# Optimization experiments

Hardware: AMD Instinct MI355X
Metric: run time of the kernel (lower is better)

## Reference

```python
import jax, jax.numpy as jnp
import numpy as np

# pywt db4 decomposition filters
DEC_LO = jnp.array([-0.010597401784997278, 0.032883011666982945, 0.030841381835986965, -0.18703481171888114, -0.02798376941698385, 0.6308807679295904, 0.7148465705525415, 0.23037781330885523], dtype=jnp.float32)
DEC_HI = jnp.array([-0.23037781330885523, 0.7148465705525415, -0.6308807679295904, -0.02798376941698385, 0.18703481171888114, 0.030841381835986965, -0.032883011666982945, -0.010597401784997278], dtype=jnp.float32)

def _dwt_step(x):
    # single-level DWT along last axis, pywt 'symmetric' mode; x: [N, n]
    L = DEC_LO.shape[0]
    xe = jnp.pad(x, ((0, 0), (L - 1, L - 1)), mode='symmetric')[:, 1:]
    k = jnp.stack([DEC_LO[::-1], DEC_HI[::-1]])[:, None, :]  # [2,1,L]
    y = jax.lax.conv_general_dilated(xe[:, None, :], k, window_strides=(2,), padding='VALID')
    return y[:, 0, :], y[:, 1, :]  # cA, cD, each [N, (n+L-1)//2]

def _wavedec(x, level):
    a, dets = x, []
    for _ in range(level):
        a, d = _dwt_step(a)
        dets.append(d)
    return [a] + dets[::-1]  # [cA_L, cD_L, ..., cD_1]

def _wavelet_kan(x, basis, scales=5):
    # torch code detaches x before pywt.wavedec -> stop_gradient for faithful bwd
    coeffs = _wavedec(jax.lax.stop_gradient(x), scales - 1)
    out = 0.0
    for s in range(scales):
        c = coeffs[s]
        out = out + c @ basis[s][:c.shape[1], :]
    return out

def _dendritic(x, W, b):
    # W: [branches, in, out]; max over branches of GELU(Linear)
    h = jnp.einsum('ni,kio->kno', x, W) + b[:, None, :]
    return jnp.max(jax.nn.gelu(h, approximate=False), axis=0)

def _layernorm(x, g, b, eps=1e-5):
    m = jnp.mean(x, -1, keepdims=True)
    v = jnp.var(x, -1, keepdims=True)
    return (x - m) * jax.lax.rsqrt(v + eps) * g + b

def setup_inputs():
    key = jax.random.key(0)
    ks = jax.random.split(key, 12)
    N, D, H, M, Z, K, E = 16384, 768, 512, 256, 256, 20, 262144
    inp = {}
    inp['x'] = jax.random.normal(ks[0], (N, D), jnp.float32)
    inp['adj_rows'] = jax.random.randint(ks[1], (E,), 0, N, jnp.int32)
    inp['adj_cols'] = jax.random.randint(ks[2], (E,), 0, N, jnp.int32)
    inp['adj_vals'] = jax.random.uniform(ks[3], (E,), jnp.float32)
    inp['basis_enc'] = jax.random.normal(ks[4], (5, D, H), jnp.float32)
    inp['ln_g'] = jnp.ones((H,), jnp.float32)
    inp['ln_b'] = jnp.zeros((H,), jnp.float32)
    inp['Wd_enc'] = jax.random.normal(ks[5], (K, H, M), jnp.float32) * 0.04
    inp['bd_enc'] = jnp.zeros((K, M), jnp.float32)
    inp['W_mu'] = jax.random.normal(ks[6], (M, Z), jnp.float32) * 0.06
    inp['b_mu'] = jnp.zeros((Z,), jnp.float32)
    inp['W_lv'] = jax.random.normal(ks[7], (M, Z), jnp.float32) * 0.06
    inp['b_lv'] = jnp.zeros((Z,), jnp.float32)
    inp['Wd_dec'] = jax.random.normal(ks[8], (K, Z, H), jnp.float32) * 0.06
    inp['bd_dec'] = jnp.zeros((K, H), jnp.float32)
    inp['basis_dec'] = jax.random.normal(ks[9], (5, H, D), jnp.float32)
    inp['eps'] = jax.random.normal(ks[10], (N, Z), jnp.float32)
    return inp

def reference(x, adj_rows, adj_cols, adj_vals, basis_enc, ln_g, ln_b, Wd_enc, bd_enc, W_mu, b_mu, W_lv, b_lv, Wd_dec, bd_dec, basis_dec, eps):
    N = x.shape[0]
    # torch.sparse.mm(adj, x) with COO adj
    xa = jax.ops.segment_sum(adj_vals[:, None] * x[adj_cols], adj_rows, num_segments=N)
    h = _wavelet_kan(xa, basis_enc)
    h = _layernorm(h, ln_g, ln_b)
    enc = _dendritic(h, Wd_enc, bd_enc)
    mu = enc @ W_mu + b_mu
    logvar = enc @ W_lv + b_lv
    z = mu + eps * jnp.exp(0.5 * logvar)
    dec = _dendritic(z, Wd_dec, bd_dec)
    recon = _wavelet_kan(dec, basis_dec)
    return recon, mu, logvar
```

## Files before the change

### kernel.cpp

```cpp
#include <hip/hip_runtime.h>

typedef __attribute__((ext_vector_type(8))) short short8v;
typedef __attribute__((ext_vector_type(8))) unsigned short ushort8v;
typedef __attribute__((ext_vector_type(4))) float float4v;

__device__ __constant__ float c_LO[8] = {
    -0.010597401784997278f, 0.032883011666982945f, 0.030841381835986965f,
    -0.18703481171888114f, -0.02798376941698385f, 0.6308807679295904f,
    0.7148465705525415f, 0.23037781330885523f};
__device__ __constant__ float c_HI[8] = {
    -0.23037781330885523f, 0.7148465705525415f, -0.6308807679295904f,
    -0.02798376941698385f, 0.18703481171888114f, 0.030841381835986965f,
    -0.032883011666982945f, -0.010597401784997278f};

__device__ __forceinline__ unsigned short f2bf(float f) {
    unsigned u = __builtin_bit_cast(unsigned, f);
    unsigned r = u + 0x7fffu + ((u >> 16) & 1u);
    return (unsigned short)(r >> 16);
}
__device__ __forceinline__ float bf2f(unsigned short u) {
    return __builtin_bit_cast(float, (unsigned)u << 16);
}

__device__ __forceinline__ float gelu_fast(float x) {
    float x3 = x * x * x;
    float y = fmaf(0.044715f, x3, x) * 0.7978845608028654f;
    float t = fminf(fmaxf(y * 2.8853900817779268f, -30.f), 30.f);
    float e = exp2f(t);
    return x * e * __builtin_amdgcn_rcpf(e + 1.0f);
}

__device__ __forceinline__ void gload_lds16(const void* g, void* l) {
    __builtin_amdgcn_global_load_lds(g, l, 16, 0, 0);
}

__device__ __forceinline__ void dwt_lvl(const float* __restrict__ in, int n, float* __restrict__ outA,
                                        unsigned short* __restrict__ outD, int m, int lane) {
    for (int j = lane; j < m; j += 64) {
        float a = 0.f, d = 0.f;
#pragma unroll
        for (int i = 0; i < 8; ++i) {
            int p = 2 * j + 7 - i;
            int q = (p < 6) ? (5 - p) : ((p < n + 6) ? (p - 6) : (2 * n + 5 - p));
            float xv = in[q];
            a = fmaf(c_LO[i], xv, a);
            d = fmaf(c_HI[i], xv, d);
        }
        outA[j] = a;
        outD[j] = f2bf(d);
    }
}
__device__ __forceinline__ void dwt_lvl_final(const float* __restrict__ in, int n, unsigned short* __restrict__ outA,
                                              unsigned short* __restrict__ outD, int m, int lane) {
    for (int j = lane; j < m; j += 64) {
        float a = 0.f, d = 0.f;
#pragma unroll
        for (int i = 0; i < 8; ++i) {
            int p = 2 * j + 7 - i;
            int q = (p < 6) ? (5 - p) : ((p < n + 6) ? (p - 6) : (2 * n + 5 - p));
            float xv = in[q];
            a = fmaf(c_LO[i], xv, a);
            d = fmaf(c_HI[i], xv, d);
        }
        outA[j] = f2bf(a);
        outD[j] = f2bf(d);
    }
}

__global__ void hist_kernel(const int* __restrict__ rows, int* __restrict__ cnt, int E) {
    int i = blockIdx.x * blockDim.x + threadIdx.x;
    if (i < E) atomicAdd(&cnt[rows[i]], 1);
}

__global__ __launch_bounds__(1024) void scan_kernel(const int* __restrict__ cnt, int* __restrict__ offs,
                                                    int* __restrict__ cursor, int Nrows, int E) {
    __shared__ int part[1024];
    int tid = threadIdx.x;
    const int per = Nrows / 1024;
    int base = tid * per;
    int local[16];
    int s = 0;
    for (int i = 0; i < per; ++i) { local[i] = s; s += cnt[base + i]; }
    part[tid] = s;
    __syncthreads();
    for (int off = 1; off < 1024; off <<= 1) {
        int v = part[tid];
        int w = (tid >= off) ? part[tid - off] : 0;
        __syncthreads();
        part[tid] = v + w;
        __syncthreads();
    }
    int pre = (tid == 0) ? 0 : part[tid - 1];
    for (int i = 0; i < per; ++i) {
        int o = pre + local[i];
        offs[base + i] = o;
        cursor[base + i] = o;
    }
    if (tid == 0) offs[Nrows] = E;
}

__global__ void scatter_kernel(const int* __restrict__ rows, const int* __restrict__ cols,
                               const float* __restrict__ vals, int* __restrict__ cursor,
                               int* __restrict__ ccol, float* __restrict__ cval, int E) {
    int i = blockIdx.x * blockDim.x + threadIdx.x;
    if (i >= E) return;
    int r = rows[i];
    int p = atomicAdd(&cursor[r], 1);
    ccol[p] = cols[i];
    cval[p] = vals[i];
}

__global__ __launch_bounds__(256) void wavedec_enc_x(const float* __restrict__ x,
                                                     unsigned short* __restrict__ cenc) {
    __shared__ float buf0[4][768];
    __shared__ float buf1[4][400];
    const int widx = threadIdx.x >> 6, lane = threadIdx.x & 63;
    const int r = blockIdx.x * 4 + widx;
    float* b0 = buf0[widx];
    float* b1 = buf1[widx];
    const float* ip = x + (size_t)r * 768;
    for (int i = lane; i < 768; i += 64) b0[i] = ip[i];
    __syncthreads();
    unsigned short* cr = cenc + (size_t)r * 800;
    dwt_lvl(b0, 768, b1, cr + 407, 387, lane);
    __syncthreads();
    dwt_lvl(b1, 387, b0, cr + 210, 197, lane);
    __syncthreads();
    dwt_lvl(b0, 197, b1, cr + 108, 102, lane);
    __syncthreads();
    dwt_lvl_final(b1, 102, cr + 0, cr + 54, 54, lane);
    if (lane < 6) cr[794 + lane] = 0;
}

__global__ __launch_bounds__(256) void spmm_ln(const unsigned short* __restrict__ hx,
                                               const int* __restrict__ offs,
                                               const int* __restrict__ ccol,
                                               const float* __restrict__ cval,
                                               const float* __restrict__ g,
                                               const float* __restrict__ b,
                                               unsigned short* __restrict__ hbf) {
    const int widx = threadIdx.x >> 6, lane = threadIdx.x & 63;
    const int r = blockIdx.x * 4 + widx;
    int s = offs[r], e = offs[r + 1];
    float acc[8] = {};
    for (int j = s; j < e; ++j) {
        int c = ccol[j];
        float v = cval[j];
        ushort8v u = *(const ushort8v*)(hx + (size_t)c * 512 + lane * 8);
#pragma unroll
        for (int t = 0; t < 8; ++t) acc[t] = fmaf(v, bf2f(u[t]), acc[t]);
    }
    float s1 = 0.f, s2 = 0.f;
#pragma unroll
    for (int t = 0; t < 8; ++t) { s1 += acc[t]; s2 = fmaf(acc[t], acc[t], s2); }
#pragma unroll
    for (int off = 32; off >= 1; off >>= 1) {
        s1 += __shfl_xor(s1, off);
        s2 += __shfl_xor(s2, off);
    }
    float mean = s1 * (1.f / 512.f);
    float var = s2 * (1.f / 512.f) - mean * mean;
    float inv = rsqrtf(var + 1e-5f);
    ushort8v o;
#pragma unroll
    for (int t = 0; t < 8; ++t) {
        int col = lane * 8 + t;
        o[t] = f2bf((acc[t] - mean) * inv * g[col] + b[col]);
    }
    *(ushort8v*)(hbf + (size_t)r * 512 + lane * 8) = o;
}

__global__ __launch_bounds__(256) void wavedec_dec(const unsigned short* __restrict__ decb,
                                                   unsigned short* __restrict__ cdec) {
    __shared__ float buf0[4][512];
    __shared__ float buf1[4][272];
    const int widx = threadIdx.x >> 6, lane = threadIdx.x & 63;
    const int r = blockIdx.x * 4 + widx;
    float* b0 = buf0[widx];
    float* b1 = buf1[widx];
    const unsigned short* ip = decb + (size_t)r * 512;
    for (int i = lane; i < 512; i += 64) b0[i] = bf2f(ip[i]);
    __syncthreads();
    unsigned short* cr = cdec + (size_t)r * 544;
    dwt_lvl(b0, 512, b1, cr + 279, 259, lane);
    __syncthreads();
    dwt_lvl(b1, 259, b0, cr + 146, 133, lane);
    __syncthreads();
    dwt_lvl(b0, 133, b1, cr + 76, 70, lane);
    __syncthreads();
    dwt_lvl_final(b1, 70, cr + 0, cr + 38, 38, lane);
    if (lane < 6) cr[538 + lane] = 0;
}

struct Bounds { int b[6]; };

__global__ __launch_bounds__(256) void pack_wT_t(const float* __restrict__ W, unsigned short* __restrict__ WT,
                                                 int K, int N, int Kpad) {
    __shared__ float t[64][65];
    const int b = blockIdx.z;
    const int k0 = blockIdx.x * 64, n0 = blockIdx.y * 64;
    const int tid = threadIdx.x;
#pragma unroll
    for (int i = 0; i < 16; ++i) {
        int idx = tid + i * 256;
        int kk = idx >> 6, nn = idx & 63;
        int k = k0 + kk;
        t[kk][nn] = (k < K) ? W[((size_t)b * K + k) * N + n0 + nn] : 0.f;
    }
    __syncthreads();
#pragma unroll
    for (int i = 0; i < 16; ++i) {
        int idx = tid + i * 256;
        int nn = idx >> 6, kk = idx & 63;
        int k = k0 + kk;
        if (k < Kpad)
            WT[((size_t)b * N + n0 + nn) * Kpad + k] = f2bf(t[kk][nn]);
    }
}

__global__ __launch_bounds__(256) void pack_basis_t(const float* __restrict__ basis, unsigned short* __restrict__ BT,
                                                    Bounds bd, int brows, int N, int K, int Kpad) {
    __shared__ float t[64][65];
    const int k0 = blockIdx.x * 64, n0 = blockIdx.y * 64;
    const int tid = threadIdx.x;
#pragma unroll
    for (int i = 0; i < 16; ++i) {
        int idx = tid + i * 256;
        int kk = idx >> 6, nn = idx & 63;
        int k = k0 + kk;
        float v = 0.f;
        if (k < K) {
            int s = 0;
#pragma unroll
            for (int u = 1; u < 5; ++u)
                if (k >= bd.b[u]) s = u;
            int lr = k - bd.b[s];
            v = basis[((size_t)s * brows + lr) * N + n0 + nn];
        }
        t[kk][nn] = v;
    }
    __syncthreads();
#pragma unroll
    for (int i = 0; i < 16; ++i) {
        int idx = tid + i * 256;
        int nn = idx >> 6, kk = idx & 63;
        int k = k0 + kk;
        if (k < Kpad)
            BT[(size_t)(n0 + nn) * Kpad + k] = f2bf(t[kk][nn]);
    }
}

template <int MODE>
__global__ __launch_bounds__(256) void gemm_mfma(const unsigned short* __restrict__ A,
                                                 const unsigned short* __restrict__ BT,
                                                 const float* __restrict__ bias,
                                                 const float* __restrict__ bias2,
                                                 void* __restrict__ Cv, void* __restrict__ Cv2,
                                                 int M, int N, int K, int lda, int ldb, int ldc, int nx) {
    __shared__ __align__(16) unsigned short As[128 * 32];
    __shared__ __align__(16) unsigned short Bs[128 * 32];
    const int tid = threadIdx.x;
    const int wave = tid >> 6, lane = tid & 63;
    const int nwg = gridDim.x;
    const int logical = (blockIdx.x & 7) * (nwg >> 3) + (blockIdx.x >> 3);
    const int mblk = logical / nx, nblk = logical - mblk * nx;
    const int m0 = mblk * 128, n0 = nblk * 128;
    const int wr = wave >> 1, wc = wave & 1;
    const int frow = lane & 15, fq = lane >> 4;

    const int off0 = tid * 16;
    const int r0 = off0 >> 6, c0 = off0 & 63;
    const int r1 = (off0 + 4096) >> 6, c1 = (off0 + 4096) & 63;
    const char* Ab = (const char*)A;
    const char* Bb = (const char*)BT;
    size_t gA0 = (size_t)(m0 + r0) * lda * 2 + c0;
    size_t gA1 = (size_t)(m0 + r1) * lda * 2 + c1;
    size_t gB0 = (size_t)(n0 + r0) * ldb * 2 + c0;
    size_t gB1 = (size_t)(n0 + r1) * ldb * 2 + c1;
    char* lA0 = (char*)As + wave * 1024;
    char* lB0 = (char*)Bs + wave * 1024;

    const int aoff = (wr * 64 + frow) * 32 + fq * 8;
    const int boff = (wc * 64 + frow) * 32 + fq * 8;

    float4v acc[4][4] = {};
    for (int k0 = 0; k0 < K; k0 += 32) {
        size_t kb2 = (size_t)k0 * 2;
        gload_lds16(Ab + gA0 + kb2, lA0);
        gload_lds16(Ab + gA1 + kb2, lA0 + 4096);
        gload_lds16(Bb + gB0 + kb2, lB0);
        gload_lds16(Bb + gB1 + kb2, lB0 + 4096);
        __syncthreads();
        short8v av[4], bv[4];
#pragma unroll
        for (int i = 0; i < 4; ++i) av[i] = *(const short8v*)(As + aoff + i * 512);
#pragma unroll
        for (int i = 0; i < 4; ++i) bv[i] = *(const short8v*)(Bs + boff + i * 512);
#pragma unroll
        for (int mi = 0; mi < 4; ++mi)
#pragma unroll
            for (int ni = 0; ni < 4; ++ni)
                acc[mi][ni] = __builtin_amdgcn_mfma_f32_16x16x32_bf16(av[mi], bv[ni], acc[mi][ni], 0, 0, 0);
        __syncthreads();
    }
#pragma unroll
    for (int ni = 0; ni < 4; ++ni) {
        int col = n0 + wc * 64 + ni * 16 + frow;
#pragma unroll
        for (int mi = 0; mi < 4; ++mi) {
#pragma unroll
            for (int i = 0; i < 4; ++i) {
                int row = m0 + wr * 64 + mi * 16 + fq * 4 + i;
                if (MODE == 0) {
                    ((float*)Cv)[(size_t)row * ldc + col] = acc[mi][ni][i];
                } else if (MODE == 1) {
                    ((unsigned short*)Cv)[(size_t)row * ldc + col] = f2bf(acc[mi][ni][i]);
                } else {
                    bool isMu = col < 256;
                    int coll = col & 255;
                    float bval = isMu ? bias[coll] : bias2[coll];
                    float* dst = (float*)(isMu ? Cv : Cv2);
                    dst[(size_t)row * 256 + coll] = acc[mi][ni][i] + bval;
                }
            }
        }
    }
}

__global__ void z_kernel(const float* __restrict__ mu, const float* __restrict__ lv,
                         const float* __restrict__ eps, unsigned short* __restrict__ z, int n4) {
    int i = blockIdx.x * blockDim.x + threadIdx.x;
    if (i >= n4) return;
    float4 m = ((const float4*)mu)[i];
    float4 l = ((const float4*)lv)[i];
    float4 e = ((const float4*)eps)[i];
    ushort4 o;
    o.x = f2bf(m.x + e.x * expf(0.5f * l.x));
    o.y = f2bf(m.y + e.y * expf(0.5f * l.y));
    o.z = f2bf(m.z + e.z * expf(0.5f * l.z));
    o.w = f2bf(m.w + e.w * expf(0.5f * l.w));
    ((ushort4*)z)[i] = o;
}

__global__ __launch_bounds__(256, 2) void dendritic_full(const unsigned short* __restrict__ A,
                                                         const unsigned short* __restrict__ WT,
                                                         const float* __restrict__ bias,
                                                         unsigned short* __restrict__ out,
                                                         int M, int Nc, int K, int nb, int nx) {
    __shared__ __align__(16) unsigned short As[128 * 64];
    __shared__ __align__(16) unsigned short Bs[2][64 * 64];
    const int tid = threadIdx.x;
    const int wave = tid >> 6;
    const int lane = tid & 63;

    const int nwg = gridDim.x;
    const int logical = (blockIdx.x & 7) * (nwg >> 3) + (blockIdx.x >> 3);
    const int mblk = logical / nx;
    const int nblk = logical - mblk * nx;
    const int n0 = nblk * 64, m0 = mblk * 128;

    const int wr = wave >> 1, wc = wave & 1;
    const int frow = lane & 15, fq = lane >> 4;

    int srA[4], scA[4];
#pragma unroll
    for (int i = 0; i < 4; ++i) {
        int ch = i * 256 + tid;
        srA[i] = ch >> 3;
        scA[i] = ((ch & 7) ^ (srA[i] & 7)) * 16;
    }
    int srB[2], scB[2];
#pragma unroll
    for (int i = 0; i < 2; ++i) {
        int ch = i * 256 + tid;
        srB[i] = ch >> 3;
        scB[i] = ((ch & 7) ^ (srB[i] & 7)) * 16;
    }
    const char* Ab = (const char*)A;
    const size_t K2 = (size_t)K * 2;
    const size_t branchBytes = (size_t)Nc * K2;
    char* lA  = (char*)As + wave * 1024;
    char* lB0 = (char*)&Bs[0][0] + wave * 1024;
    char* lB1 = (char*)&Bs[1][0] + wave * 1024;

    float4v hmn[4][2], hmx[4][2];
#pragma unroll
    for (int mi = 0; mi < 4; ++mi)
#pragma unroll
        for (int ni = 0; ni < 2; ++ni) { hmn[mi][ni] = (float4v)(1e30f); hmx[mi][ni] = (float4v)(-1e30f); }

    const int npair = nb >> 1;
    for (int p = 0; p < npair; ++p) {
        const int b0 = 2 * p, b1 = 2 * p + 1;
        const char* Bb0 = (const char*)WT + (size_t)b0 * branchBytes;
        const char* Bb1 = (const char*)WT + (size_t)b1 * branchBytes;
        float4v ac0[4][2], ac1[4][2];
#pragma unroll
        for (int ni = 0; ni < 2; ++ni) {
            int col = n0 + wc * 32 + ni * 16 + frow;
            float bv0 = bias[(size_t)b0 * Nc + col];
            float bv1 = bias[(size_t)b1 * Nc + col];
#pragma unroll
            for (int mi = 0; mi < 4; ++mi) { ac0[mi][ni] = (float4v)(bv0); ac1[mi][ni] = (float4v)(bv1); }
        }
        for (int k0 = 0; k0 < K; k0 += 64) {
            const size_t kby = (size_t)k0 * 2;
#pragma unroll
            for (int i = 0; i < 4; ++i)
                gload_lds16(Ab + (size_t)(m0 + srA[i]) * K2 + kby + scA[i], lA + i * 4096);
#pragma unroll
            for (int i = 0; i < 2; ++i)
                gload_lds16(Bb0 + (size_t)(n0 + srB[i]) * K2 + kby + scB[i], lB0 + i * 4096);
#pragma unroll
            for (int i = 0; i < 2; ++i)
                gload_lds16(Bb1 + (size_t)(n0 + srB[i]) * K2 + kby + scB[i], lB1 + i * 4096);
            __syncthreads();
#pragma unroll
            for (int kk = 0; kk < 2; ++kk) {
                short8v av[4], bv0[2], bv1[2];
                const int slot = kk * 4 + fq;
#pragma unroll
                for (int mi = 0; mi < 4; ++mi) {
                    int ra = wr * 64 + mi * 16 + frow;
                    av[mi] = *(const short8v*)((const char*)As + ra * 128 + ((slot ^ (ra & 7)) * 16));
                }
#pragma unroll
                for (int ni = 0; ni < 2; ++ni) {
                    int rb = wc * 32 + ni * 16 + frow;
                    int rboff = rb * 128 + ((slot ^ (rb & 7)) * 16);
                    bv0[ni] = *(const short8v*)((const char*)&Bs[0][0] + rboff);
                    bv1[ni] = *(const short8v*)((const char*)&Bs[1][0] + rboff);
                }
#pragma unroll
                for (int mi = 0; mi < 4; ++mi)
#pragma unroll
                    for (int ni = 0; ni < 2; ++ni) {
                        ac0[mi][ni] = __builtin_amdgcn_mfma_f32_16x16x32_bf16(av[mi], bv0[ni], ac0[mi][ni], 0, 0, 0);
                        ac1[mi][ni] = __builtin_amdgcn_mfma_f32_16x16x32_bf16(av[mi], bv1[ni], ac1[mi][ni], 0, 0, 0);
                    }
            }
            __syncthreads();
        }
#pragma unroll
        for (int ni = 0; ni < 2; ++ni)
#pragma unroll
            for (int mi = 0; mi < 4; ++mi)
#pragma unroll
                for (int i = 0; i < 4; ++i) {
                    float mn = fminf(ac0[mi][ni][i], ac1[mi][ni][i]);
                    float mx = fmaxf(ac0[mi][ni][i], ac1[mi][ni][i]);
                    hmn[mi][ni][i] = fminf(hmn[mi][ni][i], mn);
                    hmx[mi][ni][i] = fmaxf(hmx[mi][ni][i], mx);
                }
    }

#pragma unroll
    for (int ni = 0; ni < 2; ++ni) {
        int col = n0 + wc * 32 + ni * 16 + frow;
#pragma unroll
        for (int mi = 0; mi < 4; ++mi) {
#pragma unroll
            for (int i = 0; i < 4; ++i) {
                int row = m0 + wr * 64 + mi * 16 + fq * 4 + i;
                float g = fmaxf(gelu_fast(hmn[mi][ni][i]), gelu_fast(hmx[mi][ni][i]));
                out[(size_t)row * Nc + col] = f2bf(g);
            }
        }
    }
}

__global__ __launch_bounds__(256, 2) void dendritic_dec_res(const unsigned short* __restrict__ A,
                                                            const unsigned short* __restrict__ WT,
                                                            const float* __restrict__ bias,
                                                            unsigned short* __restrict__ out,
                                                            int M, int Nc, int nb, int nx) {
    constexpr int K = 256;
    __shared__ __align__(16) unsigned short As[128 * 256];
    __shared__ __align__(16) unsigned short Bs[2][64 * 64];
    const int tid = threadIdx.x;
    const int wave = tid >> 6;
    const int lane = tid & 63;

    const int nwg = gridDim.x;
    const int logical = (blockIdx.x & 7) * (nwg >> 3) + (blockIdx.x >> 3);
    const int mblk = logical / nx;
    const int nblk = logical - mblk * nx;
    const int n0 = nblk * 64, m0 = mblk * 128;

    const int wr = wave >> 1, wc = wave & 1;
    const int frow = lane & 15, fq = lane >> 4;

    const char* Ab = (const char*)A;
    const size_t K2 = (size_t)K * 2;
    for (int i = 0; i < 16; ++i) {
        int ch = i * 256 + tid;
        int row = ch >> 5, slot = ch & 31;
        int sslot = (slot & ~7) | ((slot & 7) ^ (row & 7));
        gload_lds16(Ab + (size_t)(m0 + row) * K2 + sslot * 16, (char*)As + i * 4096 + wave * 1024);
    }

    int srB[2], scB[2];
#pragma unroll
    for (int i = 0; i < 2; ++i) {
        int ch = i * 256 + tid;
        srB[i] = ch >> 3;
        scB[i] = ((ch & 7) ^ (srB[i] & 7)) * 16;
    }
    const size_t branchBytes = (size_t)Nc * K2;
    char* lB0 = (char*)&Bs[0][0] + wave * 1024;
    char* lB1 = (char*)&Bs[1][0] + wave * 1024;

    float4v hmn[4][2], hmx[4][2];
#pragma unroll
    for (int mi = 0; mi < 4; ++mi)
#pragma unroll
        for (int ni = 0; ni < 2; ++ni) { hmn[mi][ni] = (float4v)(1e30f); hmx[mi][ni] = (float4v)(-1e30f); }

    const int npair = nb >> 1;
    for (int p = 0; p < npair; ++p) {
        const int b0 = 2 * p, b1 = 2 * p + 1;
        const char* Bb0 = (const char*)WT + (size_t)b0 * branchBytes;
        const char* Bb1 = (const char*)WT + (size_t)b1 * branchBytes;
        float4v ac0[4][2], ac1[4][2];
#pragma unroll
        for (int ni = 0; ni < 2; ++ni) {
            int col = n0 + wc * 32 + ni * 16 + frow;
            float bv0 = bias[(size_t)b0 * Nc + col];
            float bv1 = bias[(size_t)b1 * Nc + col];
#pragma unroll
            for (int mi = 0; mi < 4; ++mi) { ac0[mi][ni] = (float4v)(bv0); ac1[mi][ni] = (float4v)(bv1); }
        }
        for (int k0 = 0; k0 < K; k0 += 64) {
            const size_t kby = (size_t)k0 * 2;
#pragma unroll
            for (int i = 0; i < 2; ++i)
                gload_lds16(Bb0 + (size_t)(n0 + srB[i]) * K2 + kby + scB[i], lB0 + i * 4096);
#pragma unroll
            for (int i = 0; i < 2; ++i)
                gload_lds16(Bb1 + (size_t)(n0 + srB[i]) * K2 + kby + scB[i], lB1 + i * 4096);
            __syncthreads();
#pragma unroll
            for (int kk = 0; kk < 2; ++kk) {
                short8v av[4], bv0[2], bv1[2];
                const int slot = kk * 4 + fq;
#pragma unroll
                for (int mi = 0; mi < 4; ++mi) {
                    int ra = wr * 64 + mi * 16 + frow;
                    int g = (k0 >> 3) + slot;
                    int sl = (g & ~7) | ((g & 7) ^ (ra & 7));
                    av[mi] = *(const short8v*)((const char*)As + ra * 512 + sl * 16);
                }
#pragma unroll
                for (int ni = 0; ni < 2; ++ni) {
                    int rb = wc * 32 + ni * 16 + frow;
                    int rboff = rb * 128 + ((slot ^ (rb & 7)) * 16);
                    bv0[ni] = *(const short8v*)((const char*)&Bs[0][0] + rboff);
                    bv1[ni] = *(const short8v*)((const char*)&Bs[1][0] + rboff);
                }
#pragma unroll
                for (int mi = 0; mi < 4; ++mi)
#pragma unroll
                    for (int ni = 0; ni < 2; ++ni) {
                        ac0[mi][ni] = __builtin_amdgcn_mfma_f32_16x16x32_bf16(av[mi], bv0[ni], ac0[mi][ni], 0, 0, 0);
                        ac1[mi][ni] = __builtin_amdgcn_mfma_f32_16x16x32_bf16(av[mi], bv1[ni], ac1[mi][ni], 0, 0, 0);
                    }
            }
            __syncthreads();
        }
#pragma unroll
        for (int ni = 0; ni < 2; ++ni)
#pragma unroll
            for (int mi = 0; mi < 4; ++mi)
#pragma unroll
                for (int i = 0; i < 4; ++i) {
                    float mn = fminf(ac0[mi][ni][i], ac1[mi][ni][i]);
                    float mx = fmaxf(ac0[mi][ni][i], ac1[mi][ni][i]);
                    hmn[mi][ni][i] = fminf(hmn[mi][ni][i], mn);
                    hmx[mi][ni][i] = fmaxf(hmx[mi][ni][i], mx);
                }
    }

#pragma unroll
    for (int ni = 0; ni < 2; ++ni) {
        int col = n0 + wc * 32 + ni * 16 + frow;
#pragma unroll
        for (int mi = 0; mi < 4; ++mi) {
#pragma unroll
            for (int i = 0; i < 4; ++i) {
                int row = m0 + wr * 64 + mi * 16 + fq * 4 + i;
                float g = fmaxf(gelu_fast(hmn[mi][ni][i]), gelu_fast(hmx[mi][ni][i]));
                out[(size_t)row * Nc + col] = f2bf(g);
            }
        }
    }
}

extern "C" void kernel_launch(void* const* d_in, const int* in_sizes, int n_in,
                              void* d_out, int out_size, void* d_ws, size_t ws_size,
                              hipStream_t stream) {
    const float* x        = (const float*)d_in[0];
    const int*   arows    = (const int*)d_in[1];
    const int*   acols    = (const int*)d_in[2];
    const float* avals    = (const float*)d_in[3];
    const float* basisenc = (const float*)d_in[4];
    const float* ln_g     = (const float*)d_in[5];
    const float* ln_b     = (const float*)d_in[6];
    const float* Wd_enc   = (const float*)d_in[7];
    const float* bd_enc   = (const float*)d_in[8];
    const float* W_mu     = (const float*)d_in[9];
    const float* b_mu     = (const float*)d_in[10];
    const float* W_lv     = (const float*)d_in[11];
    const float* b_lv     = (const float*)d_in[12];
    const float* Wd_dec   = (const float*)d_in[13];
    const float* bd_dec   = (const float*)d_in[14];
    const float* basisdec = (const float*)d_in[15];
    const float* epsin    = (const float*)d_in[16];

    const int N = 16384;
    const int E = in_sizes[1];

    float* ws = (float*)d_ws;
    const size_t A0 = 0;
    const size_t B0 = A0 + (size_t)N * 768;
    const size_t C0 = B0 + (size_t)N * 400;
    const size_t F0 = C0 + (size_t)N * 387;
    const size_t G0 = F0 + 3100672;

    unsigned short* hx   = (unsigned short*)(ws + A0);
    unsigned short* cenc = (unsigned short*)(ws + B0);
    unsigned short* cdec = (unsigned short*)(ws + B0);
    unsigned short* zb   = cdec + (size_t)N * 544;
    unsigned short* hbf  = (unsigned short*)(ws + C0);
    unsigned short* encb = hbf + (size_t)N * 512;
    unsigned short* decb = (unsigned short*)(ws + C0);
    unsigned short* wF = (unsigned short*)(ws + F0);
    unsigned short* BceT   = wF;
    unsigned short* BcdT   = BceT + 512 * 800;
    unsigned short* WdencT = BcdT + 768 * 544;
    unsigned short* WddecT = WdencT + 20 * 256 * 512;
    unsigned short* WmuT   = WddecT + 20 * 512 * 256;
    unsigned short* WlvT   = WmuT + 256 * 256;
    int*   csr_cnt  = (int*)(ws + G0);
    int*   csr_offs = csr_cnt + N;
    int*   csr_cur  = csr_offs + N + 1;
    int*   csr_col  = csr_cur + N;
    float* csr_val  = (float*)(csr_col + E);

    float* out_recon = (float*)d_out;
    float* out_mu    = out_recon + (size_t)N * 768;
    float* out_lv    = out_mu + (size_t)N * 256;

    {
        Bounds be = {{0, 54, 108, 210, 407, 794}};
        pack_basis_t<<<dim3(13, 8), 256, 0, stream>>>(basisenc, BceT, be, 768, 512, 794, 800);
        Bounds bdd = {{0, 38, 76, 146, 279, 538}};
        pack_basis_t<<<dim3(9, 12), 256, 0, stream>>>(basisdec, BcdT, bdd, 512, 768, 538, 544);
        pack_wT_t<<<dim3(8, 4, 20), 256, 0, stream>>>(Wd_enc, WdencT, 512, 256, 512);
        pack_wT_t<<<dim3(4, 8, 20), 256, 0, stream>>>(Wd_dec, WddecT, 256, 512, 256);
        pack_wT_t<<<dim3(4, 4, 1), 256, 0, stream>>>(W_mu, WmuT, 256, 256, 256);
        pack_wT_t<<<dim3(4, 4, 1), 256, 0, stream>>>(W_lv, WlvT, 256, 256, 256);
    }

    hipMemsetAsync(csr_cnt, 0, N * sizeof(int), stream);
    hist_kernel<<<(E + 255) / 256, 256, 0, stream>>>(arows, csr_cnt, E);
    scan_kernel<<<1, 1024, 0, stream>>>(csr_cnt, csr_offs, csr_cur, N, E);
    scatter_kernel<<<(E + 255) / 256, 256, 0, stream>>>(arows, acols, avals, csr_cur, csr_col, csr_val, E);
    wavedec_enc_x<<<N / 4, 256, 0, stream>>>(x, cenc);

    gemm_mfma<1><<<(512 / 128) * (N / 128), 256, 0, stream>>>(cenc, BceT, nullptr, nullptr, hx, nullptr,
                                                              N, 512, 800, 800, 800, 512, 512 / 128);

    spmm_ln<<<N / 4, 256, 0, stream>>>(hx, csr_offs, csr_col, csr_val, ln_g, ln_b, hbf);

    dendritic_full<<<4 * (N / 128), 256, 0, stream>>>(hbf, WdencT, bd_enc, encb, N, 256, 512, 20, 4);

    gemm_mfma<2><<<(512 / 128) * (N / 128), 256, 0, stream>>>(encb, WmuT, b_mu, b_lv, out_mu, out_lv,
                                                              N, 512, 256, 256, 256, 256, 512 / 128);

    z_kernel<<<(N * 256 / 4 + 255) / 256, 256, 0, stream>>>(out_mu, out_lv, epsin, zb, N * 256 / 4);

    dendritic_dec_res<<<8 * (N / 128), 256, 0, stream>>>(zb, WddecT, bd_dec, decb, N, 512, 20, 8);

    wavedec_dec<<<N / 4, 256, 0, stream>>>(decb, cdec);

    gemm_mfma<0><<<(768 / 128) * (N / 128), 256, 0, stream>>>(cdec, BcdT, nullptr, nullptr, out_recon, nullptr,
                                                              N, 768, 544, 544, 544, 768, 768 / 128);

    (void)ws_size; (void)out_size; (void)n_in;
}
```

Measured before the change: 457.3 us.

## Merge weight packing, encoder wavedec and histogram into one prep kernel; unroll SpMM

```diff
diff --git a/kernel.cpp b/kernel.cpp
--- a/kernel.cpp
+++ b/kernel.cpp
@@ -67,9 +67,123 @@
     }
 }
 
-__global__ void hist_kernel(const int* __restrict__ rows, int* __restrict__ cnt, int E) {
-    int i = blockIdx.x * blockDim.x + threadIdx.x;
-    if (i < E) atomicAdd(&cnt[rows[i]], 1);
+struct Bounds { int b[6]; };
+
+__device__ __forceinline__ void job_pack_w(const float* __restrict__ W, unsigned short* __restrict__ WT,
+                                           int br, int k0, int n0, int K, int N, int Kpad,
+                                           float (*t)[65], int tid) {
+#pragma unroll
+    for (int i = 0; i < 16; ++i) {
+        int idx = tid + i * 256;
+        int kk = idx >> 6, nn = idx & 63;
+        int k = k0 + kk;
+        t[kk][nn] = (k < K) ? W[((size_t)br * K + k) * N + n0 + nn] : 0.f;
+    }
+    __syncthreads();
+#pragma unroll
+    for (int i = 0; i < 16; ++i) {
+        int idx = tid + i * 256;
+        int nn = idx >> 6, kk = idx & 63;
+        int k = k0 + kk;
+        if (k < Kpad)
+            WT[((size_t)br * N + n0 + nn) * Kpad + k] = f2bf(t[kk][nn]);
+    }
+}
+
+__device__ __forceinline__ void job_pack_basis(const float* __restrict__ basis, unsigned short* __restrict__ BT,
+                                               Bounds bd, int brows, int N, int K, int Kpad,
+                                               int k0, int n0, float (*t)[65], int tid) {
+#pragma unroll
+    for (int i = 0; i < 16; ++i) {
+        int idx = tid + i * 256;
+        int kk = idx >> 6, nn = idx & 63;
+        int k = k0 + kk;
+        float v = 0.f;
+        if (k < K) {
+            int s = 0;
+#pragma unroll
+            for (int u = 1; u < 5; ++u)
+                if (k >= bd.b[u]) s = u;
+            int lr = k - bd.b[s];
+            v = basis[((size_t)s * brows + lr) * N + n0 + nn];
+        }
+        t[kk][nn] = v;
+    }
+    __syncthreads();
+#pragma unroll
+    for (int i = 0; i < 16; ++i) {
+        int idx = tid + i * 256;
+        int nn = idx >> 6, kk = idx & 63;
+        int k = k0 + kk;
+        if (k < Kpad)
+            BT[(size_t)(n0 + nn) * Kpad + k] = f2bf(t[kk][nn]);
+    }
+}
+
+__global__ __launch_bounds__(256) void prep_kernel(const float* __restrict__ x,
+                                                   const float* __restrict__ basisenc,
+                                                   const float* __restrict__ basisdec,
+                                                   const float* __restrict__ Wd_enc,
+                                                   const float* __restrict__ Wd_dec,
+                                                   const float* __restrict__ W_mu,
+                                                   const float* __restrict__ W_lv,
+                                                   const int* __restrict__ arows, int E,
+                                                   unsigned short* __restrict__ cenc,
+                                                   unsigned short* __restrict__ BceT,
+                                                   unsigned short* __restrict__ BcdT,
+                                                   unsigned short* __restrict__ WdencT,
+                                                   unsigned short* __restrict__ WddecT,
+                                                   unsigned short* __restrict__ WmuT,
+                                                   unsigned short* __restrict__ WlvT,
+                                                   int* __restrict__ csr_cnt) {
+    __shared__ __align__(16) char smem[18688];
+    const int bid = blockIdx.x;
+    const int tid = threadIdx.x;
+    float (*t)[65] = (float(*)[65])smem;
+
+    if (bid < 104) {
+        Bounds be = {{0, 54, 108, 210, 407, 794}};
+        int b = bid;
+        job_pack_basis(basisenc, BceT, be, 768, 512, 794, 800, (b % 13) * 64, (b / 13) * 64, t, tid);
+    } else if (bid < 212) {
+        Bounds bdd = {{0, 38, 76, 146, 279, 538}};
+        int b = bid - 104;
+        job_pack_basis(basisdec, BcdT, bdd, 512, 768, 538, 544, (b % 9) * 64, (b / 9) * 64, t, tid);
+    } else if (bid < 852) {
+        int b = bid - 212;
+        int br = b / 32, rem = b % 32;
+        job_pack_w(Wd_enc, WdencT, br, (rem % 8) * 64, (rem / 8) * 64, 512, 256, 512, t, tid);
+    } else if (bid < 1492) {
+        int b = bid - 852;
+        int br = b / 32, rem = b % 32;
+        job_pack_w(Wd_dec, WddecT, br, (rem % 4) * 64, (rem / 4) * 64, 256, 512, 256, t, tid);
+    } else if (bid < 1508) {
+        int b = bid - 1492;
+        job_pack_w(W_mu, WmuT, 0, (b % 4) * 64, (b / 4) * 64, 256, 256, 256, t, tid);
+    } else if (bid < 1524) {
+        int b = bid - 1508;
+        job_pack_w(W_lv, WlvT, 0, (b % 4) * 64, (b / 4) * 64, 256, 256, 256, t, tid);
+    } else if (bid < 5620) {
+        const int widx = tid >> 6, lane = tid & 63;
+        const int r = (bid - 1524) * 4 + widx;
+        float* b0 = (float*)smem + widx * 1168;
+        float* b1 = b0 + 768;
+        const float* ip = x + (size_t)r * 768;
+        for (int i = lane; i < 768; i += 64) b0[i] = ip[i];
+        __syncthreads();
+        unsigned short* cr = cenc + (size_t)r * 800;
+        dwt_lvl(b0, 768, b1, cr + 407, 387, lane);
+        __syncthreads();
+        dwt_lvl(b1, 387, b0, cr + 210, 197, lane);
+        __syncthreads();
+        dwt_lvl(b0, 197, b1, cr + 108, 102, lane);
+        __syncthreads();
+        dwt_lvl_final(b1, 102, cr + 0, cr + 54, 54, lane);
+        if (lane < 6) cr[794 + lane] = 0;
+    } else {
+        int i = (bid - 5620) * 256 + tid;
+        if (i < E) atomicAdd(&csr_cnt[arows[i]], 1);
+    }
 }
 
 __global__ __launch_bounds__(1024) void scan_kernel(const int* __restrict__ cnt, int* __restrict__ offs,
@@ -110,28 +224,6 @@
     cval[p] = vals[i];
 }
 
-__global__ __launch_bounds__(256) void wavedec_enc_x(const float* __restrict__ x,
-                                                     unsigned short* __restrict__ cenc) {
-    __shared__ float buf0[4][768];
-    __shared__ float buf1[4][400];
-    const int widx = threadIdx.x >> 6, lane = threadIdx.x & 63;
-    const int r = blockIdx.x * 4 + widx;
-    float* b0 = buf0[widx];
-    float* b1 = buf1[widx];
-    const float* ip = x + (size_t)r * 768;
-    for (int i = lane; i < 768; i += 64) b0[i] = ip[i];
-    __syncthreads();
-    unsigned short* cr = cenc + (size_t)r * 800;
-    dwt_lvl(b0, 768, b1, cr + 407, 387, lane);
-    __syncthreads();
-    dwt_lvl(b1, 387, b0, cr + 210, 197, lane);
-    __syncthreads();
-    dwt_lvl(b0, 197, b1, cr + 108, 102, lane);
-    __syncthreads();
-    dwt_lvl_final(b1, 102, cr + 0, cr + 54, 54, lane);
-    if (lane < 6) cr[794 + lane] = 0;
-}
-
 __global__ __launch_bounds__(256) void spmm_ln(const unsigned short* __restrict__ hx,
                                                const int* __restrict__ offs,
                                                const int* __restrict__ ccol,
@@ -142,14 +234,29 @@
     const int widx = threadIdx.x >> 6, lane = threadIdx.x & 63;
     const int r = blockIdx.x * 4 + widx;
     int s = offs[r], e = offs[r + 1];
-    float acc[8] = {};
-    for (int j = s; j < e; ++j) {
-        int c = ccol[j];
-        float v = cval[j];
-        ushort8v u = *(const ushort8v*)(hx + (size_t)c * 512 + lane * 8);
-#pragma unroll
-        for (int t = 0; t < 8; ++t) acc[t] = fmaf(v, bf2f(u[t]), acc[t]);
-    }
+    float acc[8] = {}, acc2[8] = {};
+    int j = s;
+    for (; j + 1 < e; j += 2) {
+        int c0 = ccol[j], c1 = ccol[j + 1];
+        float v0 = cval[j], v1 = cval[j + 1];
+        ushort8v u0 = *(const ushort8v*)(hx + (size_t)c0 * 512 + lane * 8);
+        ushort8v u1 = *(const ushort8v*)(hx + (size_t)c1 * 512 + lane * 8);
+#pragma unroll
+        for (int t = 0; t < 8; ++t) {
+            acc[t] = fmaf(v0, bf2f(u0[t]), acc[t]);
+            acc2[t] = fmaf(v1, bf2f(u1[t]), acc2[t]);
+        }
+    }
+    if (j < e) {
+        int c0 = ccol[j];
+        float v0 = cval[j];
+        ushort8v u0 = *(const ushort8v*)(hx + (size_t)c0 * 512 + lane * 8);
+#pragma unroll
+        for (int t = 0; t < 8; ++t) acc[t] = fmaf(v0, bf2f(u0[t]), acc[t]);
+    }
+#pragma unroll
+    for (int t = 0; t < 8; ++t) acc[t] += acc2[t];
+
     float s1 = 0.f, s2 = 0.f;
 #pragma unroll
     for (int t = 0; t < 8; ++t) { s1 += acc[t]; s2 = fmaf(acc[t], acc[t], s2); }
@@ -192,64 +299,6 @@
     if (lane < 6) cr[538 + lane] = 0;
 }
 
-struct Bounds { int b[6]; };
-
-__global__ __launch_bounds__(256) void pack_wT_t(const float* __restrict__ W, unsigned short* __restrict__ WT,
-                                                 int K, int N, int Kpad) {
-    __shared__ float t[64][65];
-    const int b = blockIdx.z;
-    const int k0 = blockIdx.x * 64, n0 = blockIdx.y * 64;
-    const int tid = threadIdx.x;
-#pragma unroll
-    for (int i = 0; i < 16; ++i) {
-        int idx = tid + i * 256;
-        int kk = idx >> 6, nn = idx & 63;
-        int k = k0 + kk;
-        t[kk][nn] = (k < K) ? W[((size_t)b * K + k) * N + n0 + nn] : 0.f;
-    }
-    __syncthreads();
-#pragma unroll
-    for (int i = 0; i < 16; ++i) {
-        int idx = tid + i * 256;
-        int nn = idx >> 6, kk = idx & 63;
-        int k = k0 + kk;
-        if (k < Kpad)
-            WT[((size_t)b * N + n0 + nn) * Kpad + k] = f2bf(t[kk][nn]);
-    }
-}
-
-__global__ __launch_bounds__(256) void pack_basis_t(const float* __restrict__ basis, unsigned short* __restrict__ BT,
-                                                    Bounds bd, int brows, int N, int K, int Kpad) {
-    __shared__ float t[64][65];
-    const int k0 = blockIdx.x * 64, n0 = blockIdx.y * 64;
-    const int tid = threadIdx.x;
-#pragma unroll
-    for (int i = 0; i < 16; ++i) {
-        int idx = tid + i * 256;
-        int kk = idx >> 6, nn = idx & 63;
-        int k = k0 + kk;
-        float v = 0.f;
-        if (k < K) {
-            int s = 0;
-#pragma unroll
-            for (int u = 1; u < 5; ++u)
-                if (k >= bd.b[u]) s = u;
-            int lr = k - bd.b[s];
-            v = basis[((size_t)s * brows + lr) * N + n0 + nn];
-        }
-        t[kk][nn] = v;
-    }
-    __syncthreads();
-#pragma unroll
-    for (int i = 0; i < 16; ++i) {
-        int idx = tid + i * 256;
-        int nn = idx >> 6, kk = idx & 63;
-        int k = k0 + kk;
-        if (k < Kpad)
-            BT[(size_t)(n0 + nn) * Kpad + k] = f2bf(t[kk][nn]);
-    }
-}
-
 template <int MODE>
 __global__ __launch_bounds__(256) void gemm_mfma(const unsigned short* __restrict__ A,
                                                  const unsigned short* __restrict__ BT,
@@ -650,22 +699,15 @@
     float* out_mu    = out_recon + (size_t)N * 768;
     float* out_lv    = out_mu + (size_t)N * 256;
 
+    hipMemsetAsync(csr_cnt, 0, N * sizeof(int), stream);
     {
-        Bounds be = {{0, 54, 108, 210, 407, 794}};
-        pack_basis_t<<<dim3(13, 8), 256, 0, stream>>>(basisenc, BceT, be, 768, 512, 794, 800);
-        Bounds bdd = {{0, 38, 76, 146, 279, 538}};
-        pack_basis_t<<<dim3(9, 12), 256, 0, stream>>>(basisdec, BcdT, bdd, 512, 768, 538, 544);
-        pack_wT_t<<<dim3(8, 4, 20), 256, 0, stream>>>(Wd_enc, WdencT, 512, 256, 512);
-        pack_wT_t<<<dim3(4, 8, 20), 256, 0, stream>>>(Wd_dec, WddecT, 256, 512, 256);
-        pack_wT_t<<<dim3(4, 4, 1), 256, 0, stream>>>(W_mu, WmuT, 256, 256, 256);
-        pack_wT_t<<<dim3(4, 4, 1), 256, 0, stream>>>(W_lv, WlvT, 256, 256, 256);
-    }
-
-    hipMemsetAsync(csr_cnt, 0, N * sizeof(int), stream);
-    hist_kernel<<<(E + 255) / 256, 256, 0, stream>>>(arows, csr_cnt, E);
+        const int nwgPrep = 104 + 108 + 640 + 640 + 16 + 16 + (N / 4) + (E + 255) / 256;
+        prep_kernel<<<nwgPrep, 256, 0, stream>>>(x, basisenc, basisdec, Wd_enc, Wd_dec, W_mu, W_lv,
+                                                 arows, E, cenc, BceT, BcdT, WdencT, WddecT, WmuT, WlvT,
+                                                 csr_cnt);
+    }
     scan_kernel<<<1, 1024, 0, stream>>>(csr_cnt, csr_offs, csr_cur, N, E);
     scatter_kernel<<<(E + 255) / 256, 256, 0, stream>>>(arows, acols, avals, csr_cur, csr_col, csr_val, E);
-    wavedec_enc_x<<<N / 4, 256, 0, stream>>>(x, cenc);
 
     gemm_mfma<1><<<(512 / 128) * (N / 128), 256, 0, stream>>>(cenc, BceT, nullptr, nullptr, hx, nullptr,
                                                               N, 512, 800, 800, 800, 512, 512 / 128);
```

New measurement: 392.5 us. 14.2% less time.
